# Kernel tuning notes

Measured on AMD Instinct MI355X. Metric: run time of the kernel, lower is better.

Reference implementation:

```python
import jax, jax.numpy as jnp
import numpy as np

D_MODEL = 512
WINDOW = 128
N_HEADS = 8


def setup_inputs() -> dict:
    key = jax.random.key(0)
    k1, k2, k3, k4, k5 = jax.random.split(key, 5)
    B, S, D = 8, 4096, D_MODEL
    scale = 1.0 / np.sqrt(D)
    return {
        "x": jax.random.normal(k1, (B, S, D), dtype=jnp.float32),
        "in_proj_w": jax.random.normal(k2, (3 * D, D), dtype=jnp.float32) * scale,
        "in_proj_b": jax.random.normal(k3, (3 * D,), dtype=jnp.float32) * 0.02,
        "out_proj_w": jax.random.normal(k4, (D, D), dtype=jnp.float32) * scale,
        "out_proj_b": jax.random.normal(k5, (D,), dtype=jnp.float32) * 0.02,
    }


def reference(x, in_proj_w, in_proj_b, out_proj_w, out_proj_b):
    # Non-overlapping sliding-window MHA with shared weights per window.
    B, S, D = x.shape
    W = WINDOW
    H = N_HEADS
    hd = D // H
    nw = S // W  # S chosen divisible by window size

    xw = x.reshape(B, nw, W, D)
    # Fused QKV projection (torch in_proj_weight layout: [3D, D], y = x @ W^T + b)
    qkv = jnp.einsum("bnwd,ed->bnwe", xw, in_proj_w) + in_proj_b  # [B,nw,W,3D]
    q, k, v = jnp.split(qkv, 3, axis=-1)

    def to_heads(t):
        return t.reshape(B, nw, W, H, hd)

    q = to_heads(q) * (1.0 / np.sqrt(hd))
    k = to_heads(k)
    v = to_heads(v)

    # Block-diagonal attention: scores only within each window [B,nw,H,W,W]
    scores = jnp.einsum("bnqhd,bnkhd->bnhqk", q, k)
    attn = jax.nn.softmax(scores, axis=-1)
    ctx = jnp.einsum("bnhqk,bnkhd->bnqhd", attn, v)  # [B,nw,W,H,hd]
    ctx = ctx.reshape(B, S, D)

    out = jnp.einsum("bsd,ed->bse", ctx, out_proj_w) + out_proj_b
    return out
```

## Files before the change

### kernel.cpp

```cpp
#include <hip/hip_runtime.h>


typedef __bf16 bf16x8 __attribute__((ext_vector_type(8)));
typedef __bf16 bf16x4 __attribute__((ext_vector_type(4)));
typedef float  f32x4  __attribute__((ext_vector_type(4)));

#define MFMA16(a, b, c) __builtin_amdgcn_mfma_f32_16x16x32_bf16((a), (b), (c), 0, 0, 0)

#define VMCNT_(n) asm volatile("s_waitcnt vmcnt(" #n ")" ::: "memory")
#define VMCNT(n) VMCNT_(n)
#define SBAR() do { __builtin_amdgcn_sched_barrier(0); \
                    __builtin_amdgcn_s_barrier(); \
                    __builtin_amdgcn_sched_barrier(0); } while (0)

__device__ __forceinline__ void gload_lds16(const __bf16* g, void* l) {
    __builtin_amdgcn_global_load_lds(
        (const __attribute__((address_space(1))) unsigned int*)g,
        (__attribute__((address_space(3))) unsigned int*)l, 16, 0, 0);
}

__device__ __forceinline__ void cvt8(const float* __restrict__ s,
                                     __bf16* __restrict__ d, long i) {
    const float4* s4 = reinterpret_cast<const float4*>(s);
    float4 a = s4[2 * i], b = s4[2 * i + 1];
    bf16x8 v;
    v[0] = (__bf16)a.x; v[1] = (__bf16)a.y; v[2] = (__bf16)a.z; v[3] = (__bf16)a.w;
    v[4] = (__bf16)b.x; v[5] = (__bf16)b.y; v[6] = (__bf16)b.z; v[7] = (__bf16)b.w;
    *reinterpret_cast<bf16x8*>(d + 8 * i) = v;
}

__global__ void convert_k(const float* __restrict__ x,
                          const float* __restrict__ w_in,
                          const float* __restrict__ w_out,
                          __bf16* __restrict__ x_bf,
                          __bf16* __restrict__ w_in_bf,
                          __bf16* __restrict__ w_out_bf)
{
    long i0 = (long)blockIdx.x * blockDim.x + threadIdx.x;
    long stride = (long)gridDim.x * blockDim.x;
    for (long i = i0; i < 16777216 / 8; i += stride) cvt8(x, x_bf, i);
    for (long i = i0; i < 786432 / 8;   i += stride) cvt8(w_in, w_in_bf, i);
    for (long i = i0; i < 262144 / 8;   i += stride) cvt8(w_out, w_out_bf, i);
}

template<int EPI, int NN>
__global__ __launch_bounds__(512, 2)
void gemm256(const __bf16* __restrict__ A,
             const __bf16* __restrict__ Bw,
             const float* __restrict__ bias,
             void* __restrict__ Cq,
             __bf16* __restrict__ vT)
{
    __shared__ __bf16 Al[4][8192];
    __shared__ __bf16 Bl[4][8192];

    const int nwg = gridDim.x;
    const int chunk = nwg >> 3;
    const int bid = blockIdx.x;
    const int wg = (bid & 7) * chunk + (bid >> 3);
    const int nidx = wg % NN;
    const int midx = wg / NN;
    const long mbase = (long)midx * 256;
    const int colbase = nidx * 256;

    const int tid = threadIdx.x;
    const int w = tid >> 6, lane = tid & 63;
    const int lrow = lane & 15, hi = lane >> 4;
    const int wm = w >> 2, wn = w & 3;

    const int st_row = lane >> 2;
    const int st_k = 8 * ((lane & 3) ^ ((lane >> 3) & 3));
    const int rd_off = 16 * (hi ^ ((lrow >> 1) & 3));

    const __bf16* PA = A  + (mbase + w * 16 + st_row) * 512 + st_k;
    const __bf16* PB = Bw + ((long)colbase + w * 16 + st_row) * 512 + st_k;
    const int lds_w = w * 1024;

    f32x4 acc[8][4];
    #pragma unroll
    for (int rt = 0; rt < 8; ++rt)
        #pragma unroll
        for (int ct = 0; ct < 4; ++ct) acc[rt][ct] = (f32x4){0.f, 0.f, 0.f, 0.f};

    auto stageA = [&](int tt) {
        char* As = (char*)Al[tt & 3];
        gload_lds16(PA + tt * 32,             As + lds_w);
        gload_lds16(PA + 128 * 512 + tt * 32, As + 8192 + lds_w);
    };
    auto stageB = [&](int tt) {
        char* Bs = (char*)Bl[tt & 3];
        gload_lds16(PB + tt * 32,             Bs + lds_w);
        gload_lds16(PB + 128 * 512 + tt * 32, Bs + 8192 + lds_w);
    };

    bf16x8 af[4], bfr[4];
#define TILE_BODY(T, DO_STG, DO_VM, VMC)                                          \
    {                                                                             \
        const char* As = (const char*)Al[(T) & 3];                                \
        const char* Bs = (const char*)Bl[(T) & 3];                                \
                     \
        _Pragma("unroll")                                                         \
        for (int rt = 0; rt < 4; ++rt) {                                          \
            int row = 128 * wm + 16 * rt + lrow;                                  \
            af[rt] = *reinterpret_cast<const bf16x8*>(As + row * 64 + rd_off);    \
        }                                                                         \
        _Pragma("unroll")                                                         \
        for (int ct = 0; ct < 4; ++ct) {                                          \
            int row = 64 * wn + 16 * ct + lrow;                                   \
            bfr[ct] = *reinterpret_cast<const bf16x8*>(Bs + row * 64 + rd_off);   \
        }                                                                         \
        if (DO_STG) stageA((T) + 3);                                              \
        SBAR();                                                                   \
        __builtin_amdgcn_s_setprio(1);                                            \
        _Pragma("unroll")                                                         \
        for (int rt = 0; rt < 4; ++rt)                                            \
            _Pragma("unroll")                                                     \
            for (int ct = 0; ct < 4; ++ct)                                        \
                acc[rt][ct] = MFMA16(af[rt], bfr[ct], acc[rt][ct]);               \
        __builtin_amdgcn_s_setprio(0);                                            \
        SBAR();                                                                   \
                         \
        _Pragma("unroll")                                                         \
        for (int rt = 0; rt < 4; ++rt) {                                          \
            int row = 128 * wm + 64 + 16 * rt + lrow;                             \
            af[rt] = *reinterpret_cast<const bf16x8*>(As + row * 64 + rd_off);    \
        }                                                                         \
        if (DO_STG) stageB((T) + 3);                                              \
        SBAR();                                                                   \
        __builtin_amdgcn_s_setprio(1);                                            \
        _Pragma("unroll")                                                         \
        for (int rt = 0; rt < 4; ++rt)                                            \
            _Pragma("unroll")                                                     \
            for (int ct = 0; ct < 4; ++ct)                                        \
                acc[4 + rt][ct] = MFMA16(af[rt], bfr[ct], acc[4 + rt][ct]);       \
        __builtin_amdgcn_s_setprio(0);                                            \
        if (DO_VM) { VMCNT(VMC); }                                                \
        SBAR();                                                                   \
    }

    stageA(0); stageB(0); stageA(1); stageB(1); stageA(2); stageB(2);
    VMCNT(8);
    SBAR();

    #pragma unroll 1
    for (int t = 0; t < 13; ++t) TILE_BODY(t, 1, 1, 8);
    TILE_BODY(13, 0, 1, 4);
    TILE_BODY(14, 0, 1, 0);
    TILE_BODY(15, 0, 0, 0);
#undef TILE_BODY

    if (EPI == 0) {
        const int region = colbase >> 9;
        if (region < 2) {
            __bf16* qk = (__bf16*)Cq;
            const float scale = (region == 0) ? 0.125f : 1.0f;
            #pragma unroll
            for (int ct = 0; ct < 4; ++ct) {
                int colg = colbase + 64 * wn + 16 * ct + lrow;
                float b = bias[colg];
                #pragma unroll
                for (int rt = 0; rt < 8; ++rt) {
                    long row = mbase + 128 * wm + 16 * rt + 4 * hi;
                    #pragma unroll
                    for (int r = 0; r < 4; ++r)
                        qk[(row + r) * 1024 + colg] = (__bf16)((acc[rt][ct][r] + b) * scale);
                }
            }
        } else {
            #pragma unroll
            for (int ct = 0; ct < 4; ++ct) {
                int colg = colbase + 64 * wn + 16 * ct + lrow;
                float b = bias[colg];
                int e2 = colg - 1024;
                int h = e2 >> 6, d = e2 & 63;
                #pragma unroll
                for (int rt = 0; rt < 8; ++rt) {
                    long row = mbase + 128 * wm + 16 * rt + 4 * hi;
                    int win = (int)(row >> 7), tok0 = (int)(row & 127);
                    bf16x4 pk;
                    pk[0] = (__bf16)(acc[rt][ct][0] + b);
                    pk[1] = (__bf16)(acc[rt][ct][1] + b);
                    pk[2] = (__bf16)(acc[rt][ct][2] + b);
                    pk[3] = (__bf16)(acc[rt][ct][3] + b);
                    *reinterpret_cast<bf16x4*>(
                        vT + (((long)win * 8 + h) * 64 + d) * 128 + tok0) = pk;
                }
            }
        }
    } else {
        float* out = (float*)Cq;
        #pragma unroll
        for (int ct = 0; ct < 4; ++ct) {
            int colg = colbase + 64 * wn + 16 * ct + lrow;
            float b = bias[colg];
            #pragma unroll
            for (int rt = 0; rt < 8; ++rt) {
                long row = mbase + 128 * wm + 16 * rt + 4 * hi;
                #pragma unroll
                for (int r = 0; r < 4; ++r)
                    out[(row + r) * 512 + colg] = acc[rt][ct][r] + b;
            }
        }
    }
}

__global__ __launch_bounds__(256)
void swa_attn(const __bf16* __restrict__ qk,
              const __bf16* __restrict__ vT,
              __bf16* __restrict__ ctx)
{
    __shared__ __bf16 p_lds[4][32][136];

    const int bid = blockIdx.x;
    const int win = bid >> 3, h = bid & 7;
    const int tid = threadIdx.x;
    const int w = tid >> 6, lane = tid & 63;
    const int lrow = lane & 15, hi = lane >> 4;
    const long tokb = (long)win * 128;

    bf16x8 qa[2][2];
    #pragma unroll
    for (int rt = 0; rt < 2; ++rt)
        #pragma unroll
        for (int ks = 0; ks < 2; ++ks)
            qa[rt][ks] = *reinterpret_cast<const bf16x8*>(
                qk + (tokb + 32 * w + 16 * rt + lrow) * 1024 + h * 64 + ks * 32 + hi * 8);

    f32x4 s[2][8];
    #pragma unroll
    for (int rt = 0; rt < 2; ++rt)
        #pragma unroll
        for (int ct = 0; ct < 8; ++ct) s[rt][ct] = (f32x4){0.f, 0.f, 0.f, 0.f};
    #pragma unroll
    for (int ks = 0; ks < 2; ++ks) {
        #pragma unroll
        for (int ct = 0; ct < 8; ++ct) {
            bf16x8 kb = *reinterpret_cast<const bf16x8*>(
                qk + (tokb + 16 * ct + lrow) * 1024 + 512 + h * 64 + ks * 32 + hi * 8);
            s[0][ct] = MFMA16(qa[0][ks], kb, s[0][ct]);
            s[1][ct] = MFMA16(qa[1][ks], kb, s[1][ct]);
        }
    }

    float inv[2][4];
    #pragma unroll
    for (int rt = 0; rt < 2; ++rt) {
        #pragma unroll
        for (int r = 0; r < 4; ++r) {
            float m = s[rt][0][r];
            #pragma unroll
            for (int ct = 1; ct < 8; ++ct) m = fmaxf(m, s[rt][ct][r]);
            m = fmaxf(m, __shfl_xor(m, 1));
            m = fmaxf(m, __shfl_xor(m, 2));
            m = fmaxf(m, __shfl_xor(m, 4));
            m = fmaxf(m, __shfl_xor(m, 8));
            float sum = 0.f;
            #pragma unroll
            for (int ct = 0; ct < 8; ++ct) {
                float e = __expf(s[rt][ct][r] - m);
                sum += e;
                p_lds[w][16 * rt + 4 * hi + r][16 * ct + lrow] = (__bf16)e;
            }
            sum += __shfl_xor(sum, 1);
            sum += __shfl_xor(sum, 2);
            sum += __shfl_xor(sum, 4);
            sum += __shfl_xor(sum, 8);
            inv[rt][r] = 1.f / sum;
        }
    }

    f32x4 o[2][4];
    #pragma unroll
    for (int rt = 0; rt < 2; ++rt)
        #pragma unroll
        for (int ct = 0; ct < 4; ++ct) o[rt][ct] = (f32x4){0.f, 0.f, 0.f, 0.f};
    const __bf16* vb = vT + ((long)win * 8 + h) * 64 * 128;
    #pragma unroll
    for (int kt = 0; kt < 4; ++kt) {
        bf16x8 pa0 = *reinterpret_cast<const bf16x8*>(&p_lds[w][lrow][32 * kt + 8 * hi]);
        bf16x8 pa1 = *reinterpret_cast<const bf16x8*>(&p_lds[w][16 + lrow][32 * kt + 8 * hi]);
        #pragma unroll
        for (int ct = 0; ct < 4; ++ct) {
            bf16x8 vf = *reinterpret_cast<const bf16x8*>(
                vb + (16 * ct + lrow) * 128 + 32 * kt + 8 * hi);
            o[0][ct] = MFMA16(pa0, vf, o[0][ct]);
            o[1][ct] = MFMA16(pa1, vf, o[1][ct]);
        }
    }

    #pragma unroll
    for (int rt = 0; rt < 2; ++rt)
        #pragma unroll
        for (int ct = 0; ct < 4; ++ct)
            #pragma unroll
            for (int r = 0; r < 4; ++r) {
                long tok = tokb + 32 * w + 16 * rt + 4 * hi + r;
                ctx[tok * 512 + h * 64 + 16 * ct + lrow] =
                    (__bf16)(o[rt][ct][r] * inv[rt][r]);
            }
}

extern "C" void kernel_launch(void* const* d_in, const int* in_sizes, int n_in,
                              void* d_out, int out_size, void* d_ws, size_t ws_size,
                              hipStream_t stream)
{
    const float* x     = (const float*)d_in[0];
    const float* w_in  = (const float*)d_in[1];
    const float* b_in  = (const float*)d_in[2];
    const float* w_out = (const float*)d_in[3];
    const float* b_out = (const float*)d_in[4];

    char* ws = (char*)d_ws;
    __bf16* x_bf     = (__bf16*)(ws);
    __bf16* ctx      = (__bf16*)(ws);
    __bf16* vT       = (__bf16*)(ws + 33554432);
    __bf16* w_in_bf  = (__bf16*)(ws + 67108864);
    __bf16* w_out_bf = (__bf16*)(ws + 68681728);
    __bf16* qk       = (__bf16*)d_out;

    convert_k<<<2048, 256, 0, stream>>>(x, w_in, w_out, x_bf, w_in_bf, w_out_bf);
    gemm256<0, 6><<<768, 512, 0, stream>>>(x_bf, w_in_bf, b_in, (void*)qk, vT);
    swa_attn<<<2048, 256, 0, stream>>>(qk, vT, ctx);
    gemm256<1, 2><<<256, 512, 0, stream>>>(ctx, w_out_bf, b_out, d_out, nullptr);
}
```

Before: 167.9 us.

## Collapse GEMM main loop to one barrier per K-tile with merged staging

The GEMM main loop goes from two half-tile phases, each bracketed by scheduling barriers with separate A and B staging, to one phase per K-tile. Each phase waits on vmcnt and lgkmcnt, issues a single workgroup barrier, stages all A and B loads for tile T+3, loads all eight A fragments and issues all 32 MFMAs. The aim is to cut per-tile barrier and scheduling-fence overhead and give the compiler more freedom to interleave LDS reads with MFMAs. In exchange, more fragment registers are live at once, and there is less explicit control over how global-to-LDS loads overlap with compute.

```diff
diff --git a/kernel.cpp b/kernel.cpp
--- a/kernel.cpp
+++ b/kernel.cpp
@@ -9,9 +9,7 @@
 
 #define VMCNT_(n) asm volatile("s_waitcnt vmcnt(" #n ")" ::: "memory")
 #define VMCNT(n) VMCNT_(n)
-#define SBAR() do { __builtin_amdgcn_sched_barrier(0); \
-                    __builtin_amdgcn_s_barrier(); \
-                    __builtin_amdgcn_sched_barrier(0); } while (0)
+#define LGKM0() asm volatile("s_waitcnt lgkmcnt(0)" ::: "memory")
 
 __device__ __forceinline__ void gload_lds16(const __bf16* g, void* l) {
     __builtin_amdgcn_global_load_lds(
@@ -82,25 +80,27 @@
         #pragma unroll
         for (int ct = 0; ct < 4; ++ct) acc[rt][ct] = (f32x4){0.f, 0.f, 0.f, 0.f};
 
-    auto stageA = [&](int tt) {
+    auto stage = [&](int tt) {
+        const int kk = tt * 32;
         char* As = (char*)Al[tt & 3];
-        gload_lds16(PA + tt * 32,             As + lds_w);
-        gload_lds16(PA + 128 * 512 + tt * 32, As + 8192 + lds_w);
+        char* Bs = (char*)Bl[tt & 3];
+        gload_lds16(PA + kk,             As + lds_w);
+        gload_lds16(PA + 128 * 512 + kk, As + 8192 + lds_w);
+        gload_lds16(PB + kk,             Bs + lds_w);
+        gload_lds16(PB + 128 * 512 + kk, Bs + 8192 + lds_w);
     };
-    auto stageB = [&](int tt) {
-        char* Bs = (char*)Bl[tt & 3];
-        gload_lds16(PB + tt * 32,             Bs + lds_w);
-        gload_lds16(PB + 128 * 512 + tt * 32, Bs + 8192 + lds_w);
-    };
-
-    bf16x8 af[4], bfr[4];
-#define TILE_BODY(T, DO_STG, DO_VM, VMC)                                          \
+
+#define ITER(T, VM, DO_STG)                                                       \
     {                                                                             \
+        VMCNT(VM);                                                                \
+        LGKM0();                                                                  \
+        __builtin_amdgcn_s_barrier();                                             \
+        if (DO_STG) stage((T) + 3);                                               \
         const char* As = (const char*)Al[(T) & 3];                                \
         const char* Bs = (const char*)Bl[(T) & 3];                                \
-                     \
+        bf16x8 af[8], bfr[4];                                                     \
         _Pragma("unroll")                                                         \
-        for (int rt = 0; rt < 4; ++rt) {                                          \
+        for (int rt = 0; rt < 8; ++rt) {                                          \
             int row = 128 * wm + 16 * rt + lrow;                                  \
             af[rt] = *reinterpret_cast<const bf16x8*>(As + row * 64 + rd_off);    \
         }                                                                         \
@@ -109,45 +109,23 @@
             int row = 64 * wn + 16 * ct + lrow;                                   \
             bfr[ct] = *reinterpret_cast<const bf16x8*>(Bs + row * 64 + rd_off);   \
         }                                                                         \
-        if (DO_STG) stageA((T) + 3);                                              \
-        SBAR();                                                                   \
         __builtin_amdgcn_s_setprio(1);                                            \
         _Pragma("unroll")                                                         \
-        for (int rt = 0; rt < 4; ++rt)                                            \
+        for (int rt = 0; rt < 8; ++rt)                                            \
             _Pragma("unroll")                                                     \
             for (int ct = 0; ct < 4; ++ct)                                        \
                 acc[rt][ct] = MFMA16(af[rt], bfr[ct], acc[rt][ct]);               \
         __builtin_amdgcn_s_setprio(0);                                            \
-        SBAR();                                                                   \
-                         \
-        _Pragma("unroll")                                                         \
-        for (int rt = 0; rt < 4; ++rt) {                                          \
-            int row = 128 * wm + 64 + 16 * rt + lrow;                             \
-            af[rt] = *reinterpret_cast<const bf16x8*>(As + row * 64 + rd_off);    \
-        }                                                                         \
-        if (DO_STG) stageB((T) + 3);                                              \
-        SBAR();                                                                   \
-        __builtin_amdgcn_s_setprio(1);                                            \
-        _Pragma("unroll")                                                         \
-        for (int rt = 0; rt < 4; ++rt)                                            \
-            _Pragma("unroll")                                                     \
-            for (int ct = 0; ct < 4; ++ct)                                        \
-                acc[4 + rt][ct] = MFMA16(af[rt], bfr[ct], acc[4 + rt][ct]);       \
-        __builtin_amdgcn_s_setprio(0);                                            \
-        if (DO_VM) { VMCNT(VMC); }                                                \
-        SBAR();                                                                   \
-    }
-
-    stageA(0); stageB(0); stageA(1); stageB(1); stageA(2); stageB(2);
-    VMCNT(8);
-    SBAR();
+    }
+
+    stage(0); stage(1); stage(2);
 
     #pragma unroll 1
-    for (int t = 0; t < 13; ++t) TILE_BODY(t, 1, 1, 8);
-    TILE_BODY(13, 0, 1, 4);
-    TILE_BODY(14, 0, 1, 0);
-    TILE_BODY(15, 0, 0, 0);
-#undef TILE_BODY
+    for (int t = 0; t < 13; ++t) ITER(t, 8, 1);
+    ITER(13, 8, 0);
+    ITER(14, 4, 0);
+    ITER(15, 0, 0);
+#undef ITER
 
     if (EPI == 0) {
         const int region = colbase >> 9;
```

Result: slower. 176.3 us (+5.0%).
